# Optimization experiments

Measured on AMD Instinct MI355X. Metric: run time of the kernel, lower is better.

The kernel has to match this reference:

```python
import jax, jax.numpy as jnp
import numpy as np

B, D = 8192, 1024
GATE_BIAS = 0.0
LN_EPS = 1e-5


def _layernorm(x, w, b):
    mu = jnp.mean(x, axis=-1, keepdims=True)
    var = jnp.mean(jnp.square(x - mu), axis=-1, keepdims=True)
    return (x - mu) * jax.lax.rsqrt(var + LN_EPS) * w + b


def setup_inputs() -> dict:
    key = jax.random.key(0)
    ks = jax.random.split(key, 12)
    s_in = 1.0 / np.sqrt(2 * D)  # torch Linear init scale (fan_in = 2*dim)
    return {
        "x": jax.random.normal(ks[0], (B, D), jnp.float32),
        "h": jax.random.normal(ks[1], (B, D), jnp.float32),
        "ln_w": jnp.ones((2 * D,), jnp.float32),
        "ln_b": jnp.zeros((2 * D,), jnp.float32),
        "ln2_w": jnp.ones((2 * D,), jnp.float32),
        "ln2_b": jnp.zeros((2 * D,), jnp.float32),
        "Wg": jax.random.uniform(ks[2], (5 * D, 2 * D), jnp.float32, -s_in, s_in),
        "bg": jax.random.uniform(ks[3], (5 * D,), jnp.float32, -s_in, s_in),
        "Wu": jax.random.uniform(ks[4], (D, 2 * D), jnp.float32, -s_in, s_in),
        "bu": jax.random.uniform(ks[5], (D,), jnp.float32, -s_in, s_in),
    }


def reference(x, h, ln_w, ln_b, ln2_w, ln2_b, Wg, bg, Wu, bu):
    # eval mode: dropout / dropout_mask (ones) / zoneout are identity
    inp = jnp.concatenate([x, h], axis=1)          # [B, 2D]
    inp = _layernorm(inp, ln_w, ln_b)
    gates = inp @ Wg.T + bg                        # [B, 5D]
    g0, g1, g2, g3, g4 = jnp.split(gates, 5, axis=1)
    rx = jax.nn.sigmoid(g0)
    rh = jax.nn.sigmoid(g1)
    z = jax.nn.softmax(jnp.stack([g2, g3, g4 - GATE_BIAS], axis=-1), axis=-1)  # [B, D, 3]
    inp2 = jnp.concatenate([x * rx, h * rh], axis=1)
    inp2 = _layernorm(inp2, ln2_w, ln2_b)
    u = jnp.tanh(inp2 @ Wu.T + bu)                 # [B, D]
    h_new = (jnp.stack([x, h, u], axis=-1) * z).sum(-1)
    return h_new
```

## Files before the change

kernel.cpp:

```cpp
#include <hip/hip_runtime.h>

typedef __attribute__((ext_vector_type(8))) __bf16 bf16x8;
typedef __attribute__((ext_vector_type(4))) float f32x4;

#define B_ROWS 8192
#define D_DIM  1024
#define K_DIM  2048
#define NG     5120

typedef const __attribute__((address_space(1))) void cg_void;
typedef __attribute__((address_space(3))) void lds_void;

__device__ __forceinline__ float bf2f(unsigned short u) {
    union { unsigned int ui; float f; } c; c.ui = ((unsigned int)u) << 16; return c.f;
}
__device__ __forceinline__ unsigned short f2bf(float f) {
    unsigned int u = __float_as_uint(f);
    unsigned int r = u + 0x7fffu + ((u >> 16) & 1u);
    return (unsigned short)(r >> 16);
}
__device__ __forceinline__ float sigm(float v) { return 1.0f / (1.0f + __expf(-v)); }

__global__ __launch_bounds__(256) void prep_kernel(const float* __restrict__ x, const float* __restrict__ h,
                                                   const float* __restrict__ w, const float* __restrict__ b,
                                                   unsigned short* __restrict__ outln,
                                                   const float* __restrict__ wg, const float* __restrict__ wu,
                                                   unsigned short* __restrict__ og, unsigned short* __restrict__ ou) {
    const int bid = blockIdx.x;
    const int t = threadIdx.x;
    if (bid < 8192) {
        const int row = bid;
        const float4 xv = reinterpret_cast<const float4*>(x + (size_t)row * D_DIM)[t];
        const float4 hv = reinterpret_cast<const float4*>(h + (size_t)row * D_DIM)[t];
        float s  = xv.x + xv.y + xv.z + xv.w + hv.x + hv.y + hv.z + hv.w;
        float s2 = xv.x*xv.x + xv.y*xv.y + xv.z*xv.z + xv.w*xv.w
                 + hv.x*hv.x + hv.y*hv.y + hv.z*hv.z + hv.w*hv.w;
#pragma unroll
        for (int off = 32; off > 0; off >>= 1) { s += __shfl_xor(s, off); s2 += __shfl_xor(s2, off); }
        __shared__ float red[8];
        const int wid = t >> 6, lane = t & 63;
        if (lane == 0) { red[wid] = s; red[4 + wid] = s2; }
        __syncthreads();
        s  = red[0] + red[1] + red[2] + red[3];
        s2 = red[4] + red[5] + red[6] + red[7];
        const float mu  = s * (1.0f / K_DIM);
        const float var = s2 * (1.0f / K_DIM) - mu * mu;
        const float inv = rsqrtf(var + 1e-5f);
        const float4 w0 = reinterpret_cast<const float4*>(w)[t];
        const float4 b0 = reinterpret_cast<const float4*>(b)[t];
        const float4 w1 = reinterpret_cast<const float4*>(w + D_DIM)[t];
        const float4 b1 = reinterpret_cast<const float4*>(b + D_DIM)[t];
        ushort4 o0, o1;
        o0.x = f2bf((xv.x - mu) * inv * w0.x + b0.x);
        o0.y = f2bf((xv.y - mu) * inv * w0.y + b0.y);
        o0.z = f2bf((xv.z - mu) * inv * w0.z + b0.z);
        o0.w = f2bf((xv.w - mu) * inv * w0.w + b0.w);
        o1.x = f2bf((hv.x - mu) * inv * w1.x + b1.x);
        o1.y = f2bf((hv.y - mu) * inv * w1.y + b1.y);
        o1.z = f2bf((hv.z - mu) * inv * w1.z + b1.z);
        o1.w = f2bf((hv.w - mu) * inv * w1.w + b1.w);
        reinterpret_cast<ushort4*>(outln + (size_t)row * K_DIM)[t] = o0;
        reinterpret_cast<ushort4*>(outln + (size_t)row * K_DIM + D_DIM)[t] = o1;
    } else {
        const int NG4 = 5120 * 2048 / 4;
        const int NU4 = 1024 * 2048 / 4;
        const int i = (bid - 8192) * 256 + t;
        if (i < NG4) {
            float4 v = reinterpret_cast<const float4*>(wg)[i];
            ushort4 o; o.x = f2bf(v.x); o.y = f2bf(v.y); o.z = f2bf(v.z); o.w = f2bf(v.w);
            reinterpret_cast<ushort4*>(og)[i] = o;
        } else if (i < NG4 + NU4) {
            int j = i - NG4;
            float4 v = reinterpret_cast<const float4*>(wu)[j];
            ushort4 o; o.x = f2bf(v.x); o.y = f2bf(v.y); o.z = f2bf(v.z); o.w = f2bf(v.w);
            reinterpret_cast<ushort4*>(ou)[j] = o;
        }
    }
}

__global__ __launch_bounds__(256) void gate_ln2_kernel(const float* __restrict__ x, const float* __restrict__ h,
                                                       const unsigned short* __restrict__ gates,
                                                       const float* __restrict__ w, const float* __restrict__ b,
                                                       unsigned short* __restrict__ out) {
    const int row = blockIdx.x;
    const int t = threadIdx.x;
    const float4 xv = reinterpret_cast<const float4*>(x + (size_t)row * D_DIM)[t];
    const float4 hv = reinterpret_cast<const float4*>(h + (size_t)row * D_DIM)[t];
    const ushort4 g0v = reinterpret_cast<const ushort4*>(gates + (size_t)row * NG)[t];
    const ushort4 g1v = reinterpret_cast<const ushort4*>(gates + (size_t)row * NG + D_DIM)[t];
    float a0 = xv.x * sigm(bf2f(g0v.x));
    float a1 = xv.y * sigm(bf2f(g0v.y));
    float a2 = xv.z * sigm(bf2f(g0v.z));
    float a3 = xv.w * sigm(bf2f(g0v.w));
    float c0 = hv.x * sigm(bf2f(g1v.x));
    float c1 = hv.y * sigm(bf2f(g1v.y));
    float c2 = hv.z * sigm(bf2f(g1v.z));
    float c3 = hv.w * sigm(bf2f(g1v.w));
    float s  = a0 + a1 + a2 + a3 + c0 + c1 + c2 + c3;
    float s2 = a0*a0 + a1*a1 + a2*a2 + a3*a3 + c0*c0 + c1*c1 + c2*c2 + c3*c3;
#pragma unroll
    for (int off = 32; off > 0; off >>= 1) { s += __shfl_xor(s, off); s2 += __shfl_xor(s2, off); }
    __shared__ float red[8];
    const int wid = t >> 6, lane = t & 63;
    if (lane == 0) { red[wid] = s; red[4 + wid] = s2; }
    __syncthreads();
    s  = red[0] + red[1] + red[2] + red[3];
    s2 = red[4] + red[5] + red[6] + red[7];
    const float mu  = s * (1.0f / K_DIM);
    const float var = s2 * (1.0f / K_DIM) - mu * mu;
    const float inv = rsqrtf(var + 1e-5f);
    const float4 w0 = reinterpret_cast<const float4*>(w)[t];
    const float4 b0 = reinterpret_cast<const float4*>(b)[t];
    const float4 w1 = reinterpret_cast<const float4*>(w + D_DIM)[t];
    const float4 b1 = reinterpret_cast<const float4*>(b + D_DIM)[t];
    ushort4 o0, o1;
    o0.x = f2bf((a0 - mu) * inv * w0.x + b0.x);
    o0.y = f2bf((a1 - mu) * inv * w0.y + b0.y);
    o0.z = f2bf((a2 - mu) * inv * w0.z + b0.z);
    o0.w = f2bf((a3 - mu) * inv * w0.w + b0.w);
    o1.x = f2bf((c0 - mu) * inv * w1.x + b1.x);
    o1.y = f2bf((c1 - mu) * inv * w1.y + b1.y);
    o1.z = f2bf((c2 - mu) * inv * w1.z + b1.z);
    o1.w = f2bf((c3 - mu) * inv * w1.w + b1.w);
    reinterpret_cast<ushort4*>(out + (size_t)row * K_DIM)[t] = o0;
    reinterpret_cast<ushort4*>(out + (size_t)row * K_DIM + D_DIM)[t] = o1;
}

#define PH(BUF, H, KQ, LOADB, STAGE_CODE, VMCNT_CODE) do {                                            \
    bf16x8 aF[4];                                                                                     \
    _Pragma("unroll")                                                                                 \
    for (int m = 0; m < 4; ++m)                                                                       \
        aF[m] = *reinterpret_cast<const bf16x8*>(                                                     \
            &smem[((BUF) * 2 + (H)) * 8192 + ((aRdS[m] ^ ((KQ) * 64)) >> 1)]);                        \
    if (LOADB) {                                                                                      \
        _Pragma("unroll")                                                                             \
        for (int n = 0; n < 4; ++n)                                                                   \
            bF[KQ][n] = *reinterpret_cast<const bf16x8*>(                                             \
                &smem[32768 + ((BUF) * 2 + bHalf) * 8192 + ((bRdS[n] ^ ((KQ) * 64)) >> 1)]);          \
    }                                                                                                 \
    STAGE_CODE;                                                                                       \
    VMCNT_CODE;                                                                                       \
    asm volatile("" ::: "memory");                                                                    \
    __builtin_amdgcn_s_barrier();                                                                     \
    asm volatile("" ::: "memory");                                                                    \
    __builtin_amdgcn_s_setprio(1);                                                                    \
    _Pragma("unroll")                                                                                 \
    for (int m = 0; m < 4; ++m)                                                                       \
        _Pragma("unroll")                                                                             \
        for (int n = 0; n < 4; ++n)                                                                   \
            acc[(H) * 4 + m][n] =                                                                     \
                __builtin_amdgcn_mfma_f32_16x16x32_bf16(aF[m], bF[KQ][n], acc[(H) * 4 + m][n], 0, 0, 0);\
    __builtin_amdgcn_s_setprio(0);                                                                    \
    asm volatile("" ::: "memory");                                                                    \
    __builtin_amdgcn_s_barrier();                                                                     \
    asm volatile("" ::: "memory");                                                                    \
} while (0)

#define PHH(BUF, H, KQ, LOADB, STAGE_CODE, VMCNT_CODE) do {                                           \
    bf16x8 aFh[2];                                                                                    \
    _Pragma("unroll")                                                                                 \
    for (int m = 0; m < 2; ++m)                                                                       \
        aFh[m] = *reinterpret_cast<const bf16x8*>(                                                    \
            &smem[((BUF) * 2 + (H)) * 8192 + ((aRdH[m] ^ ((KQ) * 64)) >> 1)]);                        \
    if (LOADB) {                                                                                      \
        _Pragma("unroll")                                                                             \
        for (int n = 0; n < 4; ++n)                                                                   \
            bF[KQ][n] = *reinterpret_cast<const bf16x8*>(                                             \
                &smem[32768 + ((BUF) * 2 + bHalf) * 8192 + ((bRdS[n] ^ ((KQ) * 64)) >> 1)]);          \
    }                                                                                                 \
    STAGE_CODE;                                                                                       \
    VMCNT_CODE;                                                                                      \
    asm volatile("" ::: "memory");                                                                    \
    __builtin_amdgcn_s_barrier();                                                                     \
    asm volatile("" ::: "memory");                                                                    \
    __builtin_amdgcn_s_setprio(1);                                                                    \
    _Pragma("unroll")                                                                                 \
    for (int m = 0; m < 2; ++m)                                                                       \
        _Pragma("unroll")                                                                             \
        for (int n = 0; n < 4; ++n)                                                                   \
            acch[(H) * 2 + m][n] =                                                                    \
                __builtin_amdgcn_mfma_f32_16x16x32_bf16(aFh[m], bF[KQ][n], acch[(H) * 2 + m][n], 0, 0, 0);\
    __builtin_amdgcn_s_setprio(0);                                                                    \
    asm volatile("" ::: "memory");                                                                    \
    __builtin_amdgcn_s_barrier();                                                                     \
    asm volatile("" ::: "memory");                                                                    \
} while (0)

#define VMC4 asm volatile("s_waitcnt vmcnt(4)" ::: "memory")
#define VMC3 asm volatile("s_waitcnt vmcnt(3)" ::: "memory")
#define VMC0 asm volatile("s_waitcnt vmcnt(0)" ::: "memory")
#define NOVM (void)0

__global__ __launch_bounds__(512, 2) void gemm_gates8(const unsigned short* __restrict__ A,
                                                      const unsigned short* __restrict__ W,
                                                      const float* __restrict__ bias,
                                                      unsigned short* __restrict__ C) {
    constexpr int K = K_DIM;
    constexpr int NT = K / 64;
    constexpr int NI = NT / 2;
    extern __shared__ unsigned short smem[];

    const int tid = threadIdx.x;
    const int bid = blockIdx.x;
    const int lane = tid & 63;
    const int wid = tid >> 6;
    const int wr = wid >> 2;
    const int wc = wid & 3;
    const int fr = lane & 15;
    const int kb = lane >> 4;
    const int bHalf = wc >> 1;
    const int swzl = (fr & 7) << 4;

    if (bid < 512) {
        const int swz = (bid & 7) * 64 + (bid >> 3);
        const int tm = swz >> 4;
        const int tn = swz & 15;
        const int Arow0 = tm * 256;
        const int Brow0 = tn * 256;

        int aRdS[4], bRdS[4];
#pragma unroll
        for (int m = 0; m < 4; ++m)
            aRdS[m] = (((wr * 64 + m * 16 + fr) * 128) + kb * 16) ^ swzl;
#pragma unroll
        for (int n = 0; n < 4; ++n)
            bRdS[n] = ((((wc & 1) * 64 + n * 16 + fr) * 128) + kb * 16) ^ swzl;

        size_t aSrc[2], bSrc[2];
        int ldsDst[2];
#pragma unroll
        for (int l = 0; l < 2; ++l) {
            const int off = (l * 512 + tid) * 16;
            const int r = off >> 7;
            const int offS = off ^ ((r & 7) << 4);
            const int cb = (offS & 127) >> 1;
            aSrc[l] = (size_t)(Arow0 + r) * K + cb;
            bSrc[l] = (size_t)(Brow0 + r) * K + cb;
            ldsDst[l] = (l * 512 + tid) * 8;
        }

        auto stageA = [&](int buf, int half, int kt) {
#pragma unroll
            for (int l = 0; l < 2; ++l)
                __builtin_amdgcn_global_load_lds(
                    (cg_void*)(A + aSrc[l] + (size_t)half * 128 * K + kt * 64),
                    (lds_void*)(&smem[(buf * 2 + half) * 8192 + ldsDst[l]]), 16, 0, 0);
        };
        auto stageB = [&](int buf, int half, int kt) {
#pragma unroll
            for (int l = 0; l < 2; ++l)
                __builtin_amdgcn_global_load_lds(
                    (cg_void*)(W + bSrc[l] + (size_t)half * 128 * K + kt * 64),
                    (lds_void*)(&smem[32768 + (buf * 2 + half) * 8192 + ldsDst[l]]), 16, 0, 0);
        };

        f32x4 acc[8][4] = {};

        stageA(0, 0, 0); stageA(0, 1, 0); stageB(0, 0, 0); stageB(0, 1, 0);
        stageB(1, 0, 1); stageB(1, 1, 1);
        VMC4;
        asm volatile("" ::: "memory");
        __builtin_amdgcn_s_barrier();
        asm volatile("" ::: "memory");

        for (int i = 0; i < NI; ++i) {
            const int t1 = 2 * i + 1;
            const int t2 = (2 * i + 2) & (NT - 1);
            const int t3 = (2 * i + 3) & (NT - 1);
            bf16x8 bF[2][4];
            PH(0, 0, 0, 1, { stageA(1, 0, t1); stageA(1, 1, t1); }, NOVM);
            PH(0, 0, 1, 1, ;, NOVM);
            PH(0, 1, 0, 0, { stageA(0, 0, t2); }, NOVM);
            PH(0, 1, 1, 0, { stageB(0, 0, t2); }, VMC4);
            PH(1, 0, 0, 1, { stageA(0, 1, t2); stageB(0, 1, t2); }, NOVM);
            PH(1, 0, 1, 1, ;, NOVM);
            PH(1, 1, 0, 0, { stageB(1, 0, t3); }, NOVM);
            PH(1, 1, 1, 0, { stageB(1, 1, t3); }, VMC4);
        }

        VMC0;
        asm volatile("" ::: "memory");
        __builtin_amdgcn_s_barrier();
        asm volatile("" ::: "memory");

#pragma unroll
        for (int n = 0; n < 4; ++n) {
            const int lcol = wc * 64 + n * 16 + fr;
            const float bvv = bias[Brow0 + lcol];
#pragma unroll
            for (int hh = 0; hh < 2; ++hh)
#pragma unroll
                for (int m = 0; m < 4; ++m) {
                    const int lr0 = wr * 64 + hh * 128 + m * 16 + kb * 4;
#pragma unroll
                    for (int j = 0; j < 4; ++j) {
                        const int lrow = lr0 + j;
                        const int byte = lrow * 512 + ((lcol * 2) ^ ((lrow & 7) << 4));
                        smem[byte >> 1] = f2bf(acc[hh * 4 + m][n][j] + bvv);
                    }
                }
        }
        asm volatile("" ::: "memory");
        __builtin_amdgcn_s_barrier();
        asm volatile("" ::: "memory");
#pragma unroll
        for (int k = 0; k < 16; ++k) {
            const int cid = k * 512 + tid;
            const int row = cid >> 5;
            const int c16 = cid & 31;
            const int byte = row * 512 + ((c16 * 16) ^ ((row & 7) << 4));
            bf16x8 v = *reinterpret_cast<const bf16x8*>(&smem[byte >> 1]);
            *reinterpret_cast<bf16x8*>(&C[(size_t)(Arow0 + row) * NG + Brow0 + c16 * 8]) = v;
        }
    } else {
        const int idx = bid - 512;
        const int sidx = (idx & 7) * 32 + (idx >> 3);
        const int t2i = sidx >> 1;
        const int mhalf = sidx & 1;
        const int tm = t2i >> 2;
        const int tn = 16 + (t2i & 3);
        const int Arow0 = tm * 256 + mhalf * 128;
        const int Brow0 = tn * 256;

        int aRdH[2], bRdS[4];
#pragma unroll
        for (int m = 0; m < 2; ++m)
            aRdH[m] = (((wr * 32 + m * 16 + fr) * 128) + kb * 16) ^ swzl;
#pragma unroll
        for (int n = 0; n < 4; ++n)
            bRdS[n] = ((((wc & 1) * 64 + n * 16 + fr) * 128) + kb * 16) ^ swzl;

        size_t aSrcH;
        {
            const int off = tid * 16;
            const int r = off >> 7;
            const int offS = off ^ ((r & 7) << 4);
            const int cb = (offS & 127) >> 1;
            aSrcH = (size_t)(Arow0 + r) * K + cb;
        }
        size_t bSrc[2];
        int ldsDst[2];
#pragma unroll
        for (int l = 0; l < 2; ++l) {
            const int off = (l * 512 + tid) * 16;
            const int r = off >> 7;
            const int offS = off ^ ((r & 7) << 4);
            const int cb = (offS & 127) >> 1;
            bSrc[l] = (size_t)(Brow0 + r) * K + cb;
            ldsDst[l] = (l * 512 + tid) * 8;
        }

        auto stageAH = [&](int buf, int half, int kt) {
            __builtin_amdgcn_global_load_lds(
                (cg_void*)(A + aSrcH + (size_t)half * 64 * K + kt * 64),
                (lds_void*)(&smem[(buf * 2 + half) * 8192 + tid * 8]), 16, 0, 0);
        };
        auto stageB = [&](int buf, int half, int kt) {
#pragma unroll
            for (int l = 0; l < 2; ++l)
                __builtin_amdgcn_global_load_lds(
                    (cg_void*)(W + bSrc[l] + (size_t)half * 128 * K + kt * 64),
                    (lds_void*)(&smem[32768 + (buf * 2 + half) * 8192 + ldsDst[l]]), 16, 0, 0);
        };

        f32x4 acch[4][4] = {};

        stageAH(0, 0, 0); stageAH(0, 1, 0); stageB(0, 0, 0); stageB(0, 1, 0);
        stageB(1, 0, 1); stageB(1, 1, 1);
        VMC4;
        asm volatile("" ::: "memory");
        __builtin_amdgcn_s_barrier();
        asm volatile("" ::: "memory");

        for (int i = 0; i < NI; ++i) {
            const int t1 = 2 * i + 1;
            const int t2 = (2 * i + 2) & (NT - 1);
            const int t3 = (2 * i + 3) & (NT - 1);
            bf16x8 bF[2][4];
            PHH(0, 0, 0, 1, { stageAH(1, 0, t1); stageAH(1, 1, t1); }, NOVM);
            PHH(0, 0, 1, 1, ;, NOVM);
            PHH(0, 1, 0, 0, { stageAH(0, 0, t2); }, NOVM);
            PHH(0, 1, 1, 0, { stageB(0, 0, t2); }, VMC3);
            PHH(1, 0, 0, 1, { stageAH(0, 1, t2); stageB(0, 1, t2); }, NOVM);
            PHH(1, 0, 1, 1, ;, NOVM);
            PHH(1, 1, 0, 0, { stageB(1, 0, t3); }, NOVM);
            PHH(1, 1, 1, 0, { stageB(1, 1, t3); }, VMC4);
        }

        VMC0;
        asm volatile("" ::: "memory");
        __builtin_amdgcn_s_barrier();
        asm volatile("" ::: "memory");

#pragma unroll
        for (int n = 0; n < 4; ++n) {
            const int lcol = wc * 64 + n * 16 + fr;
            const float bvv = bias[Brow0 + lcol];
#pragma unroll
            for (int hh = 0; hh < 2; ++hh)
#pragma unroll
                for (int m = 0; m < 2; ++m) {
                    const int lr0 = hh * 64 + wr * 32 + m * 16 + kb * 4;
#pragma unroll
                    for (int j = 0; j < 4; ++j) {
                        const int lrow = lr0 + j;
                        const int byte = lrow * 512 + ((lcol * 2) ^ ((lrow & 7) << 4));
                        smem[byte >> 1] = f2bf(acch[hh * 2 + m][n][j] + bvv);
                    }
                }
        }
        asm volatile("" ::: "memory");
        __builtin_amdgcn_s_barrier();
        asm volatile("" ::: "memory");
#pragma unroll
        for (int k = 0; k < 8; ++k) {
            const int cid = k * 512 + tid;
            const int row = cid >> 5;
            const int c16 = cid & 31;
            const int byte = row * 512 + ((c16 * 16) ^ ((row & 7) << 4));
            bf16x8 v = *reinterpret_cast<const bf16x8*>(&smem[byte >> 1]);
            *reinterpret_cast<bf16x8*>(&C[(size_t)(Arow0 + row) * NG + Brow0 + c16 * 8]) = v;
        }
    }
}

__global__ __launch_bounds__(256, 3) void gemm_out3(const unsigned short* __restrict__ A,
                                                    const unsigned short* __restrict__ W,
                                                    const float* __restrict__ bias,
                                                    const unsigned short* __restrict__ gates,
                                                    const float* __restrict__ x, const float* __restrict__ h,
                                                    float* __restrict__ out) {
    constexpr int K = K_DIM;
    constexpr int NTK = K / 32;
    extern __shared__ unsigned short smem[];

    const int tid = threadIdx.x;
    const int bid = blockIdx.x;
    const int swz = (bid & 7) * 64 + (bid >> 3);
    const int tn = swz & 7;
    const int tm = swz >> 3;
    const int Arow0 = tm * 128;
    const int Brow0 = tn * 128;

    const int lane = tid & 63;
    const int wid = tid >> 6;
    const int wr = wid >> 1;
    const int wc = wid & 1;
    const int fr = lane & 15;
    const int kb = lane >> 4;

    int aRd[4], bRd[4];
#pragma unroll
    for (int m = 0; m < 4; ++m) {
        const int row = wr * 64 + m * 16 + fr;
        aRd[m] = ((row >> 1) * 128 + ((((row & 1) * 64) + kb * 16) ^ (((row >> 1) & 7) << 4))) >> 1;
    }
#pragma unroll
    for (int n = 0; n < 4; ++n) {
        const int row = wc * 64 + n * 16 + fr;
        bRd[n] = ((row >> 1) * 128 + ((((row & 1) * 64) + kb * 16) ^ (((row >> 1) & 7) << 4))) >> 1;
    }

    size_t aSrcB[2], bSrcB[2];
#pragma unroll
    for (int l = 0; l < 2; ++l) {
        const int t2 = l * 256 + tid;
        const int line = t2 >> 3;
        const int inB = (t2 & 7) * 16;
        const int inBS = inB ^ ((line & 7) << 4);
        const int row = line * 2 + (inBS >> 6);
        const int col = (inBS & 63) >> 1;
        aSrcB[l] = (size_t)(Arow0 + row) * K + col;
        bSrcB[l] = (size_t)(Brow0 + row) * K + col;
    }

    auto stage = [&](int slot, int kt) {
#pragma unroll
        for (int l = 0; l < 2; ++l)
            __builtin_amdgcn_global_load_lds((cg_void*)(A + aSrcB[l] + kt * 32),
                                             (lds_void*)(&smem[slot * 4096 + (l * 256 + tid) * 8]), 16, 0, 0);
#pragma unroll
        for (int l = 0; l < 2; ++l)
            __builtin_amdgcn_global_load_lds((cg_void*)(W + bSrcB[l] + kt * 32),
                                             (lds_void*)(&smem[12288 + slot * 4096 + (l * 256 + tid) * 8]), 16, 0, 0);
    };

    f32x4 acc[4][4] = {};

    stage(0, 0); stage(1, 1);
    VMC4;
    asm volatile("" ::: "memory");
    __builtin_amdgcn_s_barrier();
    asm volatile("" ::: "memory");

    int sC = 0;
    for (int t = 0; t < NTK; ++t) {
        const int sP = (sC == 0) ? 2 : sC - 1;
        const int kt2 = (t + 2) & (NTK - 1);

        bf16x8 aF[4], bF[4];
#pragma unroll
        for (int m = 0; m < 4; ++m)
            aF[m] = *reinterpret_cast<const bf16x8*>(&smem[sC * 4096 + aRd[m]]);
#pragma unroll
        for (int n = 0; n < 4; ++n)
            bF[n] = *reinterpret_cast<const bf16x8*>(&smem[12288 + sC * 4096 + bRd[n]]);

        stage(sP, kt2);
        VMC4;
        asm volatile("" ::: "memory");
        __builtin_amdgcn_s_barrier();
        asm volatile("" ::: "memory");

        __builtin_amdgcn_s_setprio(1);
#pragma unroll
        for (int m = 0; m < 4; ++m)
#pragma unroll
            for (int n = 0; n < 4; ++n)
                acc[m][n] = __builtin_amdgcn_mfma_f32_16x16x32_bf16(aF[m], bF[n], acc[m][n], 0, 0, 0);
        __builtin_amdgcn_s_setprio(0);
        asm volatile("" ::: "memory");
        __builtin_amdgcn_s_barrier();
        asm volatile("" ::: "memory");

        sC = (sC == 2) ? 0 : sC + 1;
    }

    VMC0;
    asm volatile("" ::: "memory");
    __builtin_amdgcn_s_barrier();
    asm volatile("" ::: "memory");

    float* fsm = reinterpret_cast<float*>(smem);
#pragma unroll
    for (int n = 0; n < 4; ++n) {
        const int lcol = wc * 64 + n * 16 + fr;
        const int c = Brow0 + lcol;
        const float bvv = bias[c];
#pragma unroll
        for (int m = 0; m < 4; ++m) {
            const int lr0 = wr * 64 + m * 16 + kb * 4;
#pragma unroll
            for (int j = 0; j < 4; ++j) {
                const int lrow = lr0 + j;
                const size_t r = (size_t)Arow0 + lrow;
                const float u = tanhf(acc[m][n][j] + bvv);
                const size_t gb = r * NG + c;
                const float g2 = bf2f(gates[gb + 2 * D_DIM]);
                const float g3 = bf2f(gates[gb + 3 * D_DIM]);
                const float g4 = bf2f(gates[gb + 4 * D_DIM]);
                const float mx = fmaxf(fmaxf(g2, g3), g4);
                const float e2 = __expf(g2 - mx), e3 = __expf(g3 - mx), e4 = __expf(g4 - mx);
                const float zi = 1.0f / (e2 + e3 + e4);
                const size_t xi = r * D_DIM + c;
                const float ov = (x[xi] * e2 + h[xi] * e3 + u * e4) * zi;
                const int dw = lrow * 128 + (lcol ^ (((lrow >> 2) & 1) << 4));
                fsm[dw] = ov;
            }
        }
    }
    asm volatile("" ::: "memory");
    __builtin_amdgcn_s_barrier();
    asm volatile("" ::: "memory");

#pragma unroll
    for (int k = 0; k < 16; ++k) {
        const int cid = k * 256 + tid;
        const int row = cid >> 5;
        const int c4 = cid & 31;
        const int dw = row * 128 + ((c4 * 4) ^ (((row >> 2) & 1) << 4));
        float4 v = *reinterpret_cast<const float4*>(&fsm[dw]);
        *reinterpret_cast<float4*>(&out[(size_t)(Arow0 + row) * D_DIM + Brow0 + c4 * 4]) = v;
    }
}

extern "C" void kernel_launch(void* const* d_in, const int* in_sizes, int n_in,
                              void* d_out, int out_size, void* d_ws, size_t ws_size,
                              hipStream_t stream) {
    const float* x    = (const float*)d_in[0];
    const float* h    = (const float*)d_in[1];
    const float* ln_w = (const float*)d_in[2];
    const float* ln_b = (const float*)d_in[3];
    const float* ln2_w= (const float*)d_in[4];
    const float* ln2_b= (const float*)d_in[5];
    const float* Wg   = (const float*)d_in[6];
    const float* bg   = (const float*)d_in[7];
    const float* Wu   = (const float*)d_in[8];
    const float* bu   = (const float*)d_in[9];
    float* out = (float*)d_out;

    char* ws = (char*)d_ws;
    unsigned short* inp   = (unsigned short*)(ws);
    unsigned short* Wg_b  = (unsigned short*)(ws + 33554432);
    unsigned short* Wu_b  = (unsigned short*)(ws + 33554432 + 20971520);
    unsigned short* gates = (unsigned short*)(ws + 33554432 + 20971520 + 4194304);

    (void)hipFuncSetAttribute((const void*)gemm_gates8,
                              hipFuncAttributeMaxDynamicSharedMemorySize, 131072);
    (void)hipFuncSetAttribute((const void*)gemm_out3,
                              hipFuncAttributeMaxDynamicSharedMemorySize, 65536);

    const int nCvtBlocks = (5120 * 2048 / 4 + 1024 * 2048 / 4 + 255) / 256;
    prep_kernel<<<8192 + nCvtBlocks, 256, 0, stream>>>(x, h, ln_w, ln_b, inp, Wg, Wu, Wg_b, Wu_b);
    gemm_gates8<<<768, 512, 131072, stream>>>(inp, Wg_b, bg, gates);
    gate_ln2_kernel<<<8192, 256, 0, stream>>>(x, h, gates, ln2_w, ln2_b, inp);
    gemm_out3<<<512, 256, 65536, stream>>>(inp, Wu_b, bu, gates, x, h, out);
}
```

Baseline: 294.8 us.

## Widen second GEMM tile to 128x256 with 512-thread blocks

Measured after the change: 380.9 us. 29.2% more time.

```diff
diff --git a/kernel.cpp b/kernel.cpp
--- a/kernel.cpp
+++ b/kernel.cpp
@@ -424,7 +424,7 @@
     }
 }
 
-__global__ __launch_bounds__(256, 3) void gemm_out3(const unsigned short* __restrict__ A,
+__global__ __launch_bounds__(512, 4) void gemm_out2(const unsigned short* __restrict__ A,
                                                     const unsigned short* __restrict__ W,
                                                     const float* __restrict__ bias,
                                                     const unsigned short* __restrict__ gates,
@@ -436,16 +436,16 @@
 
     const int tid = threadIdx.x;
     const int bid = blockIdx.x;
-    const int swz = (bid & 7) * 64 + (bid >> 3);
-    const int tn = swz & 7;
-    const int tm = swz >> 3;
+    const int swz = (bid & 7) * 32 + (bid >> 3);
+    const int tm = swz >> 2;
+    const int tn = swz & 3;
     const int Arow0 = tm * 128;
-    const int Brow0 = tn * 128;
+    const int Bcol0 = tn * 256;
 
     const int lane = tid & 63;
     const int wid = tid >> 6;
-    const int wr = wid >> 1;
-    const int wc = wid & 1;
+    const int wr = wid >> 2;
+    const int wc = wid & 3;
     const int fr = lane & 15;
     const int kb = lane >> 4;
 
@@ -461,34 +461,43 @@
         bRd[n] = ((row >> 1) * 128 + ((((row & 1) * 64) + kb * 16) ^ (((row >> 1) & 7) << 4))) >> 1;
     }
 
-    size_t aSrcB[2], bSrcB[2];
+    size_t aSrcB;
+    {
+        const int line = tid >> 3;
+        const int inB = (tid & 7) * 16;
+        const int inBS = inB ^ ((line & 7) << 4);
+        const int row = line * 2 + (inBS >> 6);
+        const int col = (inBS & 63) >> 1;
+        aSrcB = (size_t)(Arow0 + row) * K + col;
+    }
+    size_t bSrcB[2];
 #pragma unroll
     for (int l = 0; l < 2; ++l) {
-        const int t2 = l * 256 + tid;
+        const int t2 = l * 512 + tid;
         const int line = t2 >> 3;
         const int inB = (t2 & 7) * 16;
         const int inBS = inB ^ ((line & 7) << 4);
         const int row = line * 2 + (inBS >> 6);
         const int col = (inBS & 63) >> 1;
-        aSrcB[l] = (size_t)(Arow0 + row) * K + col;
-        bSrcB[l] = (size_t)(Brow0 + row) * K + col;
-    }
-
-    auto stage = [&](int slot, int kt) {
-#pragma unroll
-        for (int l = 0; l < 2; ++l)
-            __builtin_amdgcn_global_load_lds((cg_void*)(A + aSrcB[l] + kt * 32),
-                                             (lds_void*)(&smem[slot * 4096 + (l * 256 + tid) * 8]), 16, 0, 0);
+        bSrcB[l] = (size_t)(Bcol0 + row) * K + col;
+    }
+
+    auto stageA = [&](int slot, int kt) {
+        __builtin_amdgcn_global_load_lds((cg_void*)(A + aSrcB + kt * 32),
+                                         (lds_void*)(&smem[slot * 4096 + tid * 8]), 16, 0, 0);
+    };
+    auto stageB = [&](int slot, int kt) {
 #pragma unroll
         for (int l = 0; l < 2; ++l)
             __builtin_amdgcn_global_load_lds((cg_void*)(W + bSrcB[l] + kt * 32),
-                                             (lds_void*)(&smem[12288 + slot * 4096 + (l * 256 + tid) * 8]), 16, 0, 0);
+                                             (lds_void*)(&smem[12288 + slot * 8192 + (l * 512 + tid) * 8]), 16, 0, 0);
     };
 
     f32x4 acc[4][4] = {};
 
-    stage(0, 0); stage(1, 1);
-    VMC4;
+    stageA(0, 0); stageB(0, 0);
+    stageA(1, 1); stageB(1, 1);
+    VMC3;
     asm volatile("" ::: "memory");
     __builtin_amdgcn_s_barrier();
     asm volatile("" ::: "memory");
@@ -504,10 +513,11 @@
             aF[m] = *reinterpret_cast<const bf16x8*>(&smem[sC * 4096 + aRd[m]]);
 #pragma unroll
         for (int n = 0; n < 4; ++n)
-            bF[n] = *reinterpret_cast<const bf16x8*>(&smem[12288 + sC * 4096 + bRd[n]]);
-
-        stage(sP, kt2);
-        VMC4;
+            bF[n] = *reinterpret_cast<const bf16x8*>(&smem[12288 + sC * 8192 + bRd[n]]);
+
+        stageA(sP, kt2);
+        stageB(sP, kt2);
+        VMC3;
         asm volatile("" ::: "memory");
         __builtin_amdgcn_s_barrier();
         asm volatile("" ::: "memory");
@@ -533,44 +543,52 @@
 
     float* fsm = reinterpret_cast<float*>(smem);
 #pragma unroll
-    for (int n = 0; n < 4; ++n) {
-        const int lcol = wc * 64 + n * 16 + fr;
-        const int c = Brow0 + lcol;
-        const float bvv = bias[c];
-#pragma unroll
-        for (int m = 0; m < 4; ++m) {
-            const int lr0 = wr * 64 + m * 16 + kb * 4;
-#pragma unroll
-            for (int j = 0; j < 4; ++j) {
-                const int lrow = lr0 + j;
-                const size_t r = (size_t)Arow0 + lrow;
-                const float u = tanhf(acc[m][n][j] + bvv);
-                const size_t gb = r * NG + c;
-                const float g2 = bf2f(gates[gb + 2 * D_DIM]);
-                const float g3 = bf2f(gates[gb + 3 * D_DIM]);
-                const float g4 = bf2f(gates[gb + 4 * D_DIM]);
-                const float mx = fmaxf(fmaxf(g2, g3), g4);
-                const float e2 = __expf(g2 - mx), e3 = __expf(g3 - mx), e4 = __expf(g4 - mx);
-                const float zi = 1.0f / (e2 + e3 + e4);
-                const size_t xi = r * D_DIM + c;
-                const float ov = (x[xi] * e2 + h[xi] * e3 + u * e4) * zi;
-                const int dw = lrow * 128 + (lcol ^ (((lrow >> 2) & 1) << 4));
-                fsm[dw] = ov;
+    for (int chunk = 0; chunk < 2; ++chunk) {
+        if ((wc >> 1) == chunk) {
+#pragma unroll
+            for (int n = 0; n < 4; ++n) {
+                const int lcol = wc * 64 + n * 16 + fr;
+                const int lcolL = lcol & 127;
+                const int c = Bcol0 + lcol;
+                const float bvv = bias[c];
+#pragma unroll
+                for (int m = 0; m < 4; ++m) {
+                    const int lr0 = wr * 64 + m * 16 + kb * 4;
+#pragma unroll
+                    for (int j = 0; j < 4; ++j) {
+                        const int lrow = lr0 + j;
+                        const size_t r = (size_t)Arow0 + lrow;
+                        const float u = tanhf(acc[m][n][j] + bvv);
+                        const size_t gb = r * NG + c;
+                        const float g2 = bf2f(gates[gb + 2 * D_DIM]);
+                        const float g3 = bf2f(gates[gb + 3 * D_DIM]);
+                        const float g4 = bf2f(gates[gb + 4 * D_DIM]);
+                        const float mx = fmaxf(fmaxf(g2, g3), g4);
+                        const float e2 = __expf(g2 - mx), e3 = __expf(g3 - mx), e4 = __expf(g4 - mx);
+                        const float zi = 1.0f / (e2 + e3 + e4);
+                        const size_t xi = r * D_DIM + c;
+                        const float ov = (x[xi] * e2 + h[xi] * e3 + u * e4) * zi;
+                        const int dw = lrow * 128 + (lcolL ^ (((lrow >> 2) & 1) << 4));
+                        fsm[dw] = ov;
+                    }
+                }
             }
         }
-    }
-    asm volatile("" ::: "memory");
-    __builtin_amdgcn_s_barrier();
-    asm volatile("" ::: "memory");
-
-#pragma unroll
-    for (int k = 0; k < 16; ++k) {
-        const int cid = k * 256 + tid;
-        const int row = cid >> 5;
-        const int c4 = cid & 31;
-        const int dw = row * 128 + ((c4 * 4) ^ (((row >> 2) & 1) << 4));
-        float4 v = *reinterpret_cast<const float4*>(&fsm[dw]);
-        *reinterpret_cast<float4*>(&out[(size_t)(Arow0 + row) * D_DIM + Brow0 + c4 * 4]) = v;
+        asm volatile("" ::: "memory");
+        __builtin_amdgcn_s_barrier();
+        asm volatile("" ::: "memory");
+#pragma unroll
+        for (int k = 0; k < 8; ++k) {
+            const int cid = k * 512 + tid;
+            const int row = cid >> 5;
+            const int c4 = cid & 31;
+            const int dw = row * 128 + ((c4 * 4) ^ (((row >> 2) & 1) << 4));
+            float4 v = *reinterpret_cast<const float4*>(&fsm[dw]);
+            *reinterpret_cast<float4*>(&out[(size_t)(Arow0 + row) * D_DIM + Bcol0 + chunk * 128 + c4 * 4]) = v;
+        }
+        asm volatile("" ::: "memory");
+        __builtin_amdgcn_s_barrier();
+        asm volatile("" ::: "memory");
     }
 }
 
@@ -597,12 +615,12 @@
 
     (void)hipFuncSetAttribute((const void*)gemm_gates8,
                               hipFuncAttributeMaxDynamicSharedMemorySize, 131072);
-    (void)hipFuncSetAttribute((const void*)gemm_out3,
-                              hipFuncAttributeMaxDynamicSharedMemorySize, 65536);
+    (void)hipFuncSetAttribute((const void*)gemm_out2,
+                              hipFuncAttributeMaxDynamicSharedMemorySize, 73728);
 
     const int nCvtBlocks = (5120 * 2048 / 4 + 1024 * 2048 / 4 + 255) / 256;
     prep_kernel<<<8192 + nCvtBlocks, 256, 0, stream>>>(x, h, ln_w, ln_b, inp, Wg, Wu, Wg_b, Wu_b);
     gemm_gates8<<<768, 512, 131072, stream>>>(inp, Wg_b, bg, gates);
     gate_ln2_kernel<<<8192, 256, 0, stream>>>(x, h, gates, ln2_w, ln2_b, inp);
-    gemm_out3<<<512, 256, 65536, stream>>>(inp, Wu_b, bu, gates, x, h, out);
+    gemm_out2<<<256, 512, 73728, stream>>>(inp, Wu_b, bu, gates, x, h, out);
 }
```
